# Optimization experiments

Hardware: AMD Instinct MI355X
Metric: run time of the kernel (lower is better)

## Reference

```python
import jax, jax.numpy as jnp
import numpy as np
import math

E = 1024   # embed_size
H = 16     # heads arg (actual per-'head' dim due to source's reshape quirk)
G = E // H # 64 head-groups (treated as heads in the source code)
FF = 4 * E


def setup_inputs() -> dict:
    key = jax.random.key(0)
    ks = jax.random.split(key, 12)
    s = 1.0 / math.sqrt(E)
    inp = {
        'x': jax.random.normal(ks[0], (2, 1024, E), dtype=jnp.float32),
        # linear weights stored as (in, out); torch Linear computes x @ W.T + b
        'Wq': jax.random.uniform(ks[1], (E, E), jnp.float32, -s, s),
        'Wk': jax.random.uniform(ks[2], (E, E), jnp.float32, -s, s),
        'Wv': jax.random.uniform(ks[3], (E, E), jnp.float32, -s, s),
        'Wo': jax.random.uniform(ks[4], (E, E), jnp.float32, -s, s),
        'bo': jax.random.uniform(ks[5], (E,), jnp.float32, -s, s),
        'W1': jax.random.uniform(ks[6], (E, FF), jnp.float32, -s, s),
        'b1': jax.random.uniform(ks[7], (FF,), jnp.float32, -s, s),
        'W2': jax.random.uniform(ks[8], (FF, E), jnp.float32, -1.0 / math.sqrt(FF), 1.0 / math.sqrt(FF)),
        'b2': jax.random.uniform(ks[9], (E,), jnp.float32, -s, s),
        'g1': jnp.ones((E,), jnp.float32), 'be1': jnp.zeros((E,), jnp.float32),
        'g2': jnp.ones((E,), jnp.float32), 'be2': jnp.zeros((E,), jnp.float32),
    }
    return inp


def _layernorm(x, g, b, eps=1e-5):
    mu = jnp.mean(x, axis=-1, keepdims=True)
    var = jnp.mean(jnp.square(x - mu), axis=-1, keepdims=True)
    return (x - mu) * jax.lax.rsqrt(var + eps) * g + b


def reference(x, Wq, Wk, Wv, Wo, bo, W1, b1, W2, b2, g1, be1, g2, be2):
    B, S, _ = x.shape
    # QKV projections; faithful to source: split E into (G=E//H groups, H dims),
    # group axis acts as the 'head' axis, per-head dim is H, scale = sqrt(H).
    def split(t):  # [B,S,E] -> [B,G,S,H]
        return t.reshape(B, S, G, H).transpose(0, 2, 1, 3)
    q = split(x @ Wq)
    k = split(x @ Wk)
    v = split(x @ Wv)
    att = jnp.einsum('bgsh,bgth->bgst', q, k) / math.sqrt(H)
    causal = jnp.tril(jnp.ones((S, S), dtype=bool))  # mask==1 above diag -> -inf
    att = jnp.where(causal, att, -jnp.inf)
    att = jax.nn.softmax(att, axis=-1)
    y = jnp.einsum('bgst,bgth->bgsh', att, v)          # [B,G,S,H]
    y = y.transpose(0, 2, 1, 3).reshape(B, S, E)
    attn_out = y @ Wo + bo
    # dropout is identity at inference
    x = _layernorm(attn_out + x, g1, be1)
    ff = jax.nn.relu(x @ W1 + b1) @ W2 + b2
    x = _layernorm(ff + x, g2, be2)
    return x
```

## Files before the change

kernel.cpp:

```cpp
#include <hip/hip_runtime.h>
#include <hip/hip_bf16.h>
#include <math.h>


#define E_DIM 1024
#define S_LEN 1024
#define B_SZ  2
#define G_HEADS 64
#define H_DIM 16
#define FF_DIM 4096
#define M_ROWS (B_SZ * S_LEN)
#define QKV_N  (3 * E_DIM)

#define QSCALE 0.36067376022224085f

#define VT_STRIDE 72
#define VT_BUF    1224

using bf16x8 = __attribute__((ext_vector_type(8))) short;
using f32x4  = __attribute__((ext_vector_type(4))) float;
using f32x16 = __attribute__((ext_vector_type(16))) float;
using ushort8 = __attribute__((ext_vector_type(8))) unsigned short;

static __device__ __forceinline__ unsigned short f2bf(float f) {
    union { float f; unsigned int u; } x; x.f = f;
    unsigned int r = x.u + 0x7fff + ((x.u >> 16) & 1);
    return (unsigned short)(r >> 16);
}
static __device__ __forceinline__ unsigned int pack2(float a, float b) {
    union { __hip_bfloat162 h; unsigned int u; } c;
    c.h = __float22bfloat162_rn(float2{a, b});
    return c.u;
}

__global__ __launch_bounds__(256) void cast_kernel(
    const float* __restrict__ X, unsigned short* __restrict__ Xb)
{
    const size_t i = ((size_t)blockIdx.x * 256 + threadIdx.x) * 8;
    float4 a = *(const float4*)(X + i);
    float4 b = *(const float4*)(X + i + 4);
    ushort8 o;
    o[0] = f2bf(a.x); o[1] = f2bf(a.y); o[2] = f2bf(a.z); o[3] = f2bf(a.w);
    o[4] = f2bf(b.x); o[5] = f2bf(b.y); o[6] = f2bf(b.z); o[7] = f2bf(b.w);
    *(ushort8*)(Xb + i) = o;
}

__global__ __launch_bounds__(256) void transpose_cast4_kernel(
    const float* __restrict__ W0, const float* __restrict__ W1_,
    const float* __restrict__ W2_, const float* __restrict__ W3_,
    unsigned short* __restrict__ Wt012, unsigned short* __restrict__ Wt3)
{
    __shared__ float tile[32][33];
    const int z = blockIdx.z;
    const float* W = (z == 0) ? W0 : (z == 1) ? W1_ : (z == 2) ? W2_ : W3_;
    unsigned short* Wo = (z < 3) ? (Wt012 + (size_t)z * E_DIM * E_DIM) : Wt3;
    const int n0 = blockIdx.x * 32, k0 = blockIdx.y * 32;
    const int t = threadIdx.x;
    const int r = t >> 3;
    const int c = (t & 7) * 4;

    float4 v = *(const float4*)(W + (size_t)(k0 + r) * E_DIM + n0 + c);
    tile[r][c] = v.x; tile[r][c + 1] = v.y; tile[r][c + 2] = v.z; tile[r][c + 3] = v.w;
    __syncthreads();

    ushort4 o;
    o.x = f2bf(tile[c + 0][r]); o.y = f2bf(tile[c + 1][r]);
    o.z = f2bf(tile[c + 2][r]); o.w = f2bf(tile[c + 3][r]);
    *(ushort4*)(Wo + (size_t)(n0 + r) * E_DIM + k0 + c) = o;
}

__global__ __launch_bounds__(256) void transpose_cast_ff_kernel(
    const float* __restrict__ W1_, const float* __restrict__ W2_,
    unsigned short* __restrict__ W1t, unsigned short* __restrict__ W2t)
{
    __shared__ float tile[32][33];
    const int z = blockIdx.z;
    const float* W = z ? W2_ : W1_;
    unsigned short* Wt = z ? W2t : W1t;
    const int N = z ? E_DIM : FF_DIM;
    const int K = z ? FF_DIM : E_DIM;
    const int n0 = (z ? blockIdx.y : blockIdx.x) * 32;
    const int k0 = (z ? blockIdx.x : blockIdx.y) * 32;
    const int t = threadIdx.x;
    const int r = t >> 3;
    const int c = (t & 7) * 4;

    float4 v = *(const float4*)(W + (size_t)(k0 + r) * N + n0 + c);
    tile[r][c] = v.x; tile[r][c + 1] = v.y; tile[r][c + 2] = v.z; tile[r][c + 3] = v.w;
    __syncthreads();

    ushort4 o;
    o.x = f2bf(tile[c + 0][r]); o.y = f2bf(tile[c + 1][r]);
    o.z = f2bf(tile[c + 2][r]); o.w = f2bf(tile[c + 3][r]);
    *(ushort4*)(Wt + (size_t)(n0 + r) * K + k0 + c) = o;
}

template<int ACT, int OUTBF, int SCALEQ>
__global__ __launch_bounds__(256) void gemm_mfma(
    const unsigned short* __restrict__ A,
    const unsigned short* __restrict__ Bt,
    const float* __restrict__ bias,
    float* __restrict__ C0, float* __restrict__ C1,
    unsigned short* __restrict__ Cb,
    int Krow, int Kchunk, int ldc)
{
    __shared__ __align__(16) unsigned short lds[2][12288];

    const int tid  = threadIdx.x;
    const int wave = tid >> 6;
    const int lane = tid & 63;
    const int wr = wave >> 1;
    const int wc = wave & 1;
    const int row0 = blockIdx.y * 128;
    const int col0 = blockIdx.x * 64;
    const int kbase = blockIdx.z * Kchunk;

    const int lr = lane & 15;
    const int lk = (lane >> 4) * 8;

    const int srow = (lane >> 2);
    const int scol = (lane & 3) * 8;

    f32x4 acc[4][2] = {};

    auto STAGE1 = [&](unsigned short* dstA, unsigned short* dstB, int k0) {
        #pragma unroll
        for (int i = 0; i < 2; ++i) {
            const int ci = wave + i * 4;
            const unsigned short* src =
                A + (size_t)(row0 + ci * 16 + srow) * Krow + k0 + scol;
            __builtin_amdgcn_global_load_lds(
                (const __attribute__((address_space(1))) void*)src,
                (__attribute__((address_space(3))) void*)(dstA + ci * 512),
                16, 0, 0);
        }
        {
            const unsigned short* src =
                Bt + (size_t)(col0 + wave * 16 + srow) * Krow + k0 + scol;
            __builtin_amdgcn_global_load_lds(
                (const __attribute__((address_space(1))) void*)src,
                (__attribute__((address_space(3))) void*)(dstB + wave * 512),
                16, 0, 0);
        }
    };
    auto STAGE = [&](int buf, int k0) {
        STAGE1(&lds[buf][0],    &lds[buf][4096],  k0);
        STAGE1(&lds[buf][6144], &lds[buf][10240], k0 + 32);
    };
    auto COMPUTE = [&](int buf, int sub) {
        const unsigned short* As = &lds[buf][sub * 6144];
        const unsigned short* Bs = As + 4096;
        bf16x8 a[4], b[2];
        #pragma unroll
        for (int mi = 0; mi < 4; ++mi)
            a[mi] = *(const bf16x8*)(As + (wr * 64 + mi * 16 + lr) * 32 + lk);
        #pragma unroll
        for (int ni = 0; ni < 2; ++ni)
            b[ni] = *(const bf16x8*)(Bs + (wc * 32 + ni * 16 + lr) * 32 + lk);
        #pragma unroll
        for (int mi = 0; mi < 4; ++mi)
            #pragma unroll
            for (int ni = 0; ni < 2; ++ni)
                acc[mi][ni] = __builtin_amdgcn_mfma_f32_16x16x32_bf16(
                    a[mi], b[ni], acc[mi][ni], 0, 0, 0);
    };

    const int nt = Kchunk >> 6;

    STAGE(0, kbase);
    asm volatile("s_waitcnt vmcnt(0)" ::: "memory");
    __builtin_amdgcn_s_barrier();

    int cur = 0;
    for (int t = 0; t < nt; ++t) {
        if (t + 1 < nt) STAGE(cur ^ 1, kbase + (t + 1) * 64);
        COMPUTE(cur, 0);
        COMPUTE(cur, 1);
        asm volatile("s_waitcnt vmcnt(0)" ::: "memory");
        __builtin_amdgcn_s_barrier();
        cur ^= 1;
    }

    float* Cw = blockIdx.z ? C1 : C0;
    #pragma unroll
    for (int mi = 0; mi < 4; ++mi) {
        #pragma unroll
        for (int ni = 0; ni < 2; ++ni) {
            const int cc  = col0 + wc * 32 + ni * 16 + (lane & 15);
            const int rr0 = row0 + wr * 64 + mi * 16 + ((lane >> 4) << 2);
            const float bv = bias ? bias[cc] : 0.f;
            #pragma unroll
            for (int j = 0; j < 4; ++j) {
                float v = acc[mi][ni][j] + bv;
                if (ACT == 1) v = fmaxf(v, 0.f);
                if (SCALEQ && cc < E_DIM) v *= QSCALE;
                if (OUTBF) Cb[(size_t)(rr0 + j) * ldc + cc] = f2bf(v);
                else       Cw[(size_t)(rr0 + j) * ldc + cc] = v;
            }
        }
    }
}

__global__ __launch_bounds__(256) void attn_kernel(
    const unsigned short* __restrict__ qkv, unsigned short* __restrict__ Yb)
{
    __shared__ __align__(16) unsigned short Ks[2][1024];
    __shared__ __align__(16) unsigned short Vt[2][VT_BUF];

    const int bi = blockIdx.x >> 7;
    const int bg = blockIdx.x & 127;
    const int g  = bg & (G_HEADS - 1);
    const int b  = bg >> 6;
    const int tid  = threadIdx.x;
    const int lane = tid & 63;
    const int l31  = lane & 31;
    const int hi   = lane >> 5;
    const int wv   = tid >> 6;
    const int tokb = b * S_LEN;

    const int cblk = 28 - 4 * bi;
    const int q0   = (cblk + wv) * 32;
    const int qrow = q0 + l31;
    const int nt64 = (cblk + 4) >> 1;

    const bf16x8 qf = *(const bf16x8*)(
        qkv + (size_t)(tokb + qrow) * QKV_N + g * H_DIM + hi * 8);

    f32x16 acc = {};
    const f32x16 fz = {};

    const int kv  = tid >> 7;
    const int h64 = (tid >> 6) & 1;
    const int skey  = h64 * 32 + (lane >> 1);
    const int shalf = lane & 1;
    const size_t sgo = (size_t)(g * H_DIM + (1 + kv) * E_DIM + shalf * 8);

    auto STAGE = [&](int buf, int t64, ushort8& vreg) {
        const unsigned short* src =
            qkv + (size_t)(tokb + t64 * 64 + skey) * QKV_N + sgo;
        if (kv == 0) {
            __builtin_amdgcn_global_load_lds(
                (const __attribute__((address_space(1))) void*)src,
                (__attribute__((address_space(3))) void*)(&Ks[buf][h64 * 512]),
                16, 0, 0);
        } else {
            vreg = *(const ushort8*)src;
        }
    };
    auto WRITE_V = [&](int buf, const ushort8& vreg) {
        if (kv == 1) {
            #pragma unroll
            for (int j = 0; j < 8; ++j)
                Vt[buf][(shalf * 8 + j) * VT_STRIDE + skey] = vreg[j];
        }
    };

    const int vrow = (l31 == 16) ? 16 : (l31 & 15);

    auto PROCESS = [&](int cur, int sub, int t0) {
        const bf16x8 kf = *(const bf16x8*)(&Ks[cur][(sub * 32 + l31) * 16 + hi * 8]);
        __builtin_amdgcn_s_setprio(1);
        f32x16 s = __builtin_amdgcn_mfma_f32_32x32x16_bf16(kf, qf, fz, 0, 0, 0);
        __builtin_amdgcn_s_setprio(0);

        float pq[16];
        if (t0 == q0) {
            #pragma unroll
            for (int r = 0; r < 16; ++r) {
                const int key = t0 + (r & 3) + 8 * (r >> 2) + 4 * hi;
                pq[r] = (key > qrow) ? 0.f : exp2f(s[r]);
            }
        } else {
            #pragma unroll
            for (int r = 0; r < 16; ++r) pq[r] = exp2f(s[r]);
        }

        unsigned int cw[8];
        #pragma unroll
        for (int r2 = 0; r2 < 8; ++r2) cw[r2] = pack2(pq[2 * r2], pq[2 * r2 + 1]);

        union { uint4 u; bf16x8 v; } pf0, pf1;
        {
            unsigned int a = cw[0], c = cw[2];
            asm volatile("v_permlane32_swap_b32 %0, %1" : "+v"(a), "+v"(c));
            pf0.u.x = a; pf0.u.z = c;
        }
        {
            unsigned int a = cw[1], c = cw[3];
            asm volatile("v_permlane32_swap_b32 %0, %1" : "+v"(a), "+v"(c));
            pf0.u.y = a; pf0.u.w = c;
        }
        {
            unsigned int a = cw[4], c = cw[6];
            asm volatile("v_permlane32_swap_b32 %0, %1" : "+v"(a), "+v"(c));
            pf1.u.x = a; pf1.u.z = c;
        }
        {
            unsigned int a = cw[5], c = cw[7];
            asm volatile("v_permlane32_swap_b32 %0, %1" : "+v"(a), "+v"(c));
            pf1.u.y = a; pf1.u.w = c;
        }

        const unsigned short* vbase =
            &Vt[cur][vrow * VT_STRIDE + sub * 32 + hi * 8];
        const bf16x8 vb0 = *(const bf16x8*)(vbase);
        const bf16x8 vb1 = *(const bf16x8*)(vbase + 16);

        __builtin_amdgcn_s_setprio(1);
        acc = __builtin_amdgcn_mfma_f32_32x32x16_bf16(pf0.v, vb0, acc, 0, 0, 0);
        acc = __builtin_amdgcn_mfma_f32_32x32x16_bf16(pf1.v, vb1, acc, 0, 0, 0);
        __builtin_amdgcn_s_setprio(0);
    };

    ushort8 vreg = {};
    STAGE(0, 0, vreg);
    if (kv == 1) {
        const int vt = tid - 128;
        Vt[vt >> 6][16 * VT_STRIDE + (vt & 63)] = 0x3F80;
    }
    WRITE_V(0, vreg);
    __syncthreads();

    int cur = 0;
    for (int t = 0; t < nt64; ++t) {
        ushort8 vnext = {};
        const bool more = (t + 1 < nt64);
        if (more) STAGE(cur ^ 1, t + 1, vnext);
        #pragma unroll
        for (int sub = 0; sub < 2; ++sub) {
            const int t0 = t * 64 + sub * 32;
            if (t0 <= q0) PROCESS(cur, sub, t0);
        }
        if (more) WRITE_V(cur ^ 1, vnext);
        asm volatile("s_waitcnt vmcnt(0) lgkmcnt(0)" ::: "memory");
        __builtin_amdgcn_s_barrier();
        cur ^= 1;
    }

    float linv[16];
    #pragma unroll
    for (int r = 0; r < 16; ++r) {
        const float lr_ = __shfl(acc[r], (hi << 5) + 16);
        linv[r] = __builtin_amdgcn_rcpf(lr_);
    }
    if (l31 < H_DIM) {
        #pragma unroll
        for (int r = 0; r < 16; ++r) {
            const int q = (r & 3) + 8 * (r >> 2) + 4 * hi;
            Yb[(size_t)(tokb + q0 + q) * E_DIM + g * H_DIM + l31] =
                f2bf(acc[r] * linv[r]);
        }
    }
}

__global__ __launch_bounds__(256) void add_ln2_kernel(
    const float* __restrict__ P0, const float* __restrict__ P1,
    const float* __restrict__ bias, const float* __restrict__ resid,
    const float* __restrict__ g, const float* __restrict__ be,
    float* __restrict__ O, unsigned short* __restrict__ Ob)
{
    const int row = blockIdx.x;
    const size_t base = (size_t)row * E_DIM;
    const int tid = threadIdx.x;

    float v[4];
    float s = 0.f;
    #pragma unroll
    for (int i = 0; i < 4; ++i) {
        int c = tid + i * 256;
        v[i] = P0[base + c] + P1[base + c] + bias[c] + resid[base + c];
        s += v[i];
    }

    __shared__ float red[256];
    red[tid] = s; __syncthreads();
    for (int st = 128; st >= 1; st >>= 1) {
        if (tid < st) red[tid] += red[tid + st];
        __syncthreads();
    }
    const float mu = red[0] * (1.f / E_DIM);
    __syncthreads();

    float s2 = 0.f;
    #pragma unroll
    for (int i = 0; i < 4; ++i) { float d = v[i] - mu; s2 += d * d; }
    red[tid] = s2; __syncthreads();
    for (int st = 128; st >= 1; st >>= 1) {
        if (tid < st) red[tid] += red[tid + st];
        __syncthreads();
    }
    const float rs = rsqrtf(red[0] * (1.f / E_DIM) + 1e-5f);

    #pragma unroll
    for (int i = 0; i < 4; ++i) {
        int c = tid + i * 256;
        float o = (v[i] - mu) * rs * g[c] + be[c];
        O[base + c] = o;
        if (Ob) Ob[base + c] = f2bf(o);
    }
}

extern "C" void kernel_launch(void* const* d_in, const int* in_sizes, int n_in,
                              void* d_out, int out_size, void* d_ws, size_t ws_size,
                              hipStream_t stream)
{
    const float* x  = (const float*)d_in[0];
    const float* Wq = (const float*)d_in[1];
    const float* Wk = (const float*)d_in[2];
    const float* Wv = (const float*)d_in[3];
    const float* Wo = (const float*)d_in[4];
    const float* bo = (const float*)d_in[5];
    const float* W1 = (const float*)d_in[6];
    const float* b1 = (const float*)d_in[7];
    const float* W2 = (const float*)d_in[8];
    const float* b2 = (const float*)d_in[9];
    const float* g1  = (const float*)d_in[10];
    const float* be1 = (const float*)d_in[11];
    const float* g2  = (const float*)d_in[12];
    const float* be2 = (const float*)d_in[13];

    char* W = (char*)d_ws;
    const size_t MB = 1024 * 1024;
    unsigned short* xb   = (unsigned short*)(W + 0 * MB);
    unsigned short* Wqkt = (unsigned short*)(W + 4 * MB);
    unsigned short* qkvb = (unsigned short*)(W + 10 * MB);
    unsigned short* yb   = (unsigned short*)(W + 22 * MB);
    unsigned short* Wot  = (unsigned short*)(W + 26 * MB);
    float* P_o0          = (float*)(W + 4 * MB);
    float* P_o1          = (float*)(W + 12 * MB);
    unsigned short* x1b  = (unsigned short*)(W + 20 * MB);
    float* x1            = (float*)(W + 28 * MB);
    unsigned short* W1t  = (unsigned short*)(W + 36 * MB);
    unsigned short* W2t  = (unsigned short*)(W + 44 * MB);
    unsigned short* ff1b = (unsigned short*)(W + 0 * MB);
    float* P_f1          = (float*)(W + 16 * MB);
    float* out           = (float*)d_out;

    dim3 blk(256);

    cast_kernel<<<dim3((M_ROWS * E_DIM) / (256 * 8)), blk, 0, stream>>>(x, xb);
    transpose_cast4_kernel<<<dim3(32, 32, 4), blk, 0, stream>>>(Wq, Wk, Wv, Wo, Wqkt, Wot);
    transpose_cast_ff_kernel<<<dim3(128, 32, 2), blk, 0, stream>>>(W1, W2, W1t, W2t);
    gemm_mfma<0, 1, 1><<<dim3(QKV_N / 64, M_ROWS / 128, 1), blk, 0, stream>>>(
        xb, Wqkt, nullptr, nullptr, nullptr, qkvb, E_DIM, E_DIM, QKV_N);
    attn_kernel<<<dim3(B_SZ * G_HEADS * 8), blk, 0, stream>>>(qkvb, yb);
    gemm_mfma<0, 0, 0><<<dim3(E_DIM / 64, M_ROWS / 128, 2), blk, 0, stream>>>(
        yb, Wot, nullptr, P_o0, P_o1, nullptr, E_DIM, E_DIM / 2, E_DIM);
    add_ln2_kernel<<<dim3(M_ROWS), blk, 0, stream>>>(P_o0, P_o1, bo, x, g1, be1, x1, x1b);
    gemm_mfma<1, 1, 0><<<dim3(FF_DIM / 64, M_ROWS / 128, 1), blk, 0, stream>>>(
        x1b, W1t, b1, nullptr, nullptr, ff1b, E_DIM, E_DIM, FF_DIM);
    gemm_mfma<0, 0, 0><<<dim3(E_DIM / 64, M_ROWS / 128, 2), blk, 0, stream>>>(
        ff1b, W2t, nullptr, out, P_f1, nullptr, FF_DIM, FF_DIM / 2, E_DIM);
    add_ln2_kernel<<<dim3(M_ROWS), blk, 0, stream>>>(out, P_f1, b2, x1, g2, be2, out, nullptr);
}
```

Before: 162.7 us.

## Merge prep kernels and drop LDS staging in attention for direct global loads

Three casting and transposing kernels become one prep kernel that dispatches on a flat block index, saving two launches. The attention kernel no longer stages K and V tiles through double-buffered shared memory with barriers. Each wave now walks only its own causal range of 32-key steps, loading K as a vector from global memory with a one-step prefetch and gathering V with scalar strided global loads. This removes block-level synchronisation and LDS traffic, but the many uncoalesced 2-byte V loads may cost more than they save.

After: 229.8 us. 1.41x slower.

```diff
diff --git a/kernel.cpp b/kernel.cpp
--- a/kernel.cpp
+++ b/kernel.cpp
@@ -14,9 +14,6 @@
 
 #define QSCALE 0.36067376022224085f
 
-#define VT_STRIDE 72
-#define VT_BUF    1224
-
 using bf16x8 = __attribute__((ext_vector_type(8))) short;
 using f32x4  = __attribute__((ext_vector_type(4))) float;
 using f32x16 = __attribute__((ext_vector_type(16))) float;
@@ -33,54 +30,48 @@
     return c.u;
 }
 
-__global__ __launch_bounds__(256) void cast_kernel(
-    const float* __restrict__ X, unsigned short* __restrict__ Xb)
+__global__ __launch_bounds__(256) void prep_kernel(
+    const float* __restrict__ x,
+    const float* __restrict__ Wq, const float* __restrict__ Wk,
+    const float* __restrict__ Wv, const float* __restrict__ Wo,
+    const float* __restrict__ W1_, const float* __restrict__ W2_,
+    unsigned short* __restrict__ xb, unsigned short* __restrict__ Wqkt,
+    unsigned short* __restrict__ Wot, unsigned short* __restrict__ W1t,
+    unsigned short* __restrict__ W2t)
 {
-    const size_t i = ((size_t)blockIdx.x * 256 + threadIdx.x) * 8;
-    float4 a = *(const float4*)(X + i);
-    float4 b = *(const float4*)(X + i + 4);
-    ushort8 o;
-    o[0] = f2bf(a.x); o[1] = f2bf(a.y); o[2] = f2bf(a.z); o[3] = f2bf(a.w);
-    o[4] = f2bf(b.x); o[5] = f2bf(b.y); o[6] = f2bf(b.z); o[7] = f2bf(b.w);
-    *(ushort8*)(Xb + i) = o;
-}
-
-__global__ __launch_bounds__(256) void transpose_cast4_kernel(
-    const float* __restrict__ W0, const float* __restrict__ W1_,
-    const float* __restrict__ W2_, const float* __restrict__ W3_,
-    unsigned short* __restrict__ Wt012, unsigned short* __restrict__ Wt3)
-{
+    const int id = blockIdx.x;
+    if (id < 1024) {
+        const size_t i = ((size_t)id * 256 + threadIdx.x) * 8;
+        float4 a = *(const float4*)(x + i);
+        float4 b = *(const float4*)(x + i + 4);
+        ushort8 o;
+        o[0] = f2bf(a.x); o[1] = f2bf(a.y); o[2] = f2bf(a.z); o[3] = f2bf(a.w);
+        o[4] = f2bf(b.x); o[5] = f2bf(b.y); o[6] = f2bf(b.z); o[7] = f2bf(b.w);
+        *(ushort8*)(xb + i) = o;
+        return;
+    }
+
     __shared__ float tile[32][33];
-    const int z = blockIdx.z;
-    const float* W = (z == 0) ? W0 : (z == 1) ? W1_ : (z == 2) ? W2_ : W3_;
-    unsigned short* Wo = (z < 3) ? (Wt012 + (size_t)z * E_DIM * E_DIM) : Wt3;
-    const int n0 = blockIdx.x * 32, k0 = blockIdx.y * 32;
-    const int t = threadIdx.x;
-    const int r = t >> 3;
-    const int c = (t & 7) * 4;
-
-    float4 v = *(const float4*)(W + (size_t)(k0 + r) * E_DIM + n0 + c);
-    tile[r][c] = v.x; tile[r][c + 1] = v.y; tile[r][c + 2] = v.z; tile[r][c + 3] = v.w;
-    __syncthreads();
-
-    ushort4 o;
-    o.x = f2bf(tile[c + 0][r]); o.y = f2bf(tile[c + 1][r]);
-    o.z = f2bf(tile[c + 2][r]); o.w = f2bf(tile[c + 3][r]);
-    *(ushort4*)(Wo + (size_t)(n0 + r) * E_DIM + k0 + c) = o;
-}
-
-__global__ __launch_bounds__(256) void transpose_cast_ff_kernel(
-    const float* __restrict__ W1_, const float* __restrict__ W2_,
-    unsigned short* __restrict__ W1t, unsigned short* __restrict__ W2t)
-{
-    __shared__ float tile[32][33];
-    const int z = blockIdx.z;
-    const float* W = z ? W2_ : W1_;
-    unsigned short* Wt = z ? W2t : W1t;
-    const int N = z ? E_DIM : FF_DIM;
-    const int K = z ? FF_DIM : E_DIM;
-    const int n0 = (z ? blockIdx.y : blockIdx.x) * 32;
-    const int k0 = (z ? blockIdx.x : blockIdx.y) * 32;
+    const float* W; unsigned short* Wt; int N, K, n0, k0;
+    if (id < 5120) {
+        const int q = id - 1024;
+        const int z = q >> 10;
+        W  = (z == 0) ? Wq : (z == 1) ? Wk : (z == 2) ? Wv : Wo;
+        Wt = (z < 3) ? (Wqkt + (size_t)z * E_DIM * E_DIM) : Wot;
+        N = E_DIM; K = E_DIM;
+        n0 = (q & 31) * 32; k0 = ((q >> 5) & 31) * 32;
+    } else {
+        const int q = id - 5120;
+        const int z = q >> 12;
+        const int qx = q & 4095;
+        const int bx = qx & 127, by = qx >> 7;
+        W  = z ? W2_ : W1_;
+        Wt = z ? W2t : W1t;
+        N  = z ? E_DIM : FF_DIM;
+        K  = z ? FF_DIM : E_DIM;
+        n0 = (z ? by : bx) * 32;
+        k0 = (z ? bx : by) * 32;
+    }
     const int t = threadIdx.x;
     const int r = t >> 3;
     const int c = (t & 7) * 4;
@@ -204,9 +195,6 @@
 __global__ __launch_bounds__(256) void attn_kernel(
     const unsigned short* __restrict__ qkv, unsigned short* __restrict__ Yb)
 {
-    __shared__ __align__(16) unsigned short Ks[2][1024];
-    __shared__ __align__(16) unsigned short Vt[2][VT_BUF];
-
     const int bi = blockIdx.x >> 7;
     const int bg = blockIdx.x & 127;
     const int g  = bg & (G_HEADS - 1);
@@ -221,44 +209,42 @@
     const int cblk = 28 - 4 * bi;
     const int q0   = (cblk + wv) * 32;
     const int qrow = q0 + l31;
-    const int nt64 = (cblk + 4) >> 1;
+    const int nsub = (q0 >> 5) + 1;
 
     const bf16x8 qf = *(const bf16x8*)(
         qkv + (size_t)(tokb + qrow) * QKV_N + g * H_DIM + hi * 8);
 
+    const unsigned short* kbase =
+        qkv + (size_t)(tokb + l31) * QKV_N + g * H_DIM + E_DIM + hi * 8;
+    const size_t KSTEP = (size_t)32 * QKV_N;
+
+    const bool isl = (l31 == 16);
+    const int vcol = l31 & 15;
+    const unsigned short* vbase =
+        qkv + (size_t)tokb * QKV_N + g * H_DIM + 2 * E_DIM + vcol;
+
     f32x16 acc = {};
     const f32x16 fz = {};
 
-    const int kv  = tid >> 7;
-    const int h64 = (tid >> 6) & 1;
-    const int skey  = h64 * 32 + (lane >> 1);
-    const int shalf = lane & 1;
-    const size_t sgo = (size_t)(g * H_DIM + (1 + kv) * E_DIM + shalf * 8);
-
-    auto STAGE = [&](int buf, int t64, ushort8& vreg) {
-        const unsigned short* src =
-            qkv + (size_t)(tokb + t64 * 64 + skey) * QKV_N + sgo;
-        if (kv == 0) {
-            __builtin_amdgcn_global_load_lds(
-                (const __attribute__((address_space(1))) void*)src,
-                (__attribute__((address_space(3))) void*)(&Ks[buf][h64 * 512]),
-                16, 0, 0);
-        } else {
-            vreg = *(const ushort8*)src;
-        }
-    };
-    auto WRITE_V = [&](int buf, const ushort8& vreg) {
-        if (kv == 1) {
-            #pragma unroll
-            for (int j = 0; j < 8; ++j)
-                Vt[buf][(shalf * 8 + j) * VT_STRIDE + skey] = vreg[j];
-        }
-    };
-
-    const int vrow = (l31 == 16) ? 16 : (l31 & 15);
-
-    auto PROCESS = [&](int cur, int sub, int t0) {
-        const bf16x8 kf = *(const bf16x8*)(&Ks[cur][(sub * 32 + l31) * 16 + hi * 8]);
+    bf16x8 kf = *(const bf16x8*)(kbase);
+
+    for (int t = 0; t < nsub; ++t) {
+        const int t0 = t * 32;
+
+        bf16x8 kf_next = kf;
+        if (t + 1 < nsub)
+            kf_next = *(const bf16x8*)(kbase + (size_t)(t + 1) * KSTEP);
+
+        union { unsigned short s2[8]; bf16x8 v; } vb0, vb1;
+        #pragma unroll
+        for (int e = 0; e < 8; ++e) {
+            const int k0_ = t0 + hi * 8 + e;
+            vb0.s2[e] = isl ? (unsigned short)0x3F80
+                            : vbase[(size_t)k0_ * QKV_N];
+            vb1.s2[e] = isl ? (unsigned short)0x3F80
+                            : vbase[(size_t)(k0_ + 16) * QKV_N];
+        }
+
         __builtin_amdgcn_s_setprio(1);
         f32x16 s = __builtin_amdgcn_mfma_f32_32x32x16_bf16(kf, qf, fz, 0, 0, 0);
         __builtin_amdgcn_s_setprio(0);
@@ -301,40 +287,12 @@
             pf1.u.y = a; pf1.u.w = c;
         }
 
-        const unsigned short* vbase =
-            &Vt[cur][vrow * VT_STRIDE + sub * 32 + hi * 8];
-        const bf16x8 vb0 = *(const bf16x8*)(vbase);
-        const bf16x8 vb1 = *(const bf16x8*)(vbase + 16);
-
         __builtin_amdgcn_s_setprio(1);
-        acc = __builtin_amdgcn_mfma_f32_32x32x16_bf16(pf0.v, vb0, acc, 0, 0, 0);
-        acc = __builtin_amdgcn_mfma_f32_32x32x16_bf16(pf1.v, vb1, acc, 0, 0, 0);
+        acc = __builtin_amdgcn_mfma_f32_32x32x16_bf16(pf0.v, vb0.v, acc, 0, 0, 0);
+        acc = __builtin_amdgcn_mfma_f32_32x32x16_bf16(pf1.v, vb1.v, acc, 0, 0, 0);
         __builtin_amdgcn_s_setprio(0);
-    };
-
-    ushort8 vreg = {};
-    STAGE(0, 0, vreg);
-    if (kv == 1) {
-        const int vt = tid - 128;
-        Vt[vt >> 6][16 * VT_STRIDE + (vt & 63)] = 0x3F80;
-    }
-    WRITE_V(0, vreg);
-    __syncthreads();
-
-    int cur = 0;
-    for (int t = 0; t < nt64; ++t) {
-        ushort8 vnext = {};
-        const bool more = (t + 1 < nt64);
-        if (more) STAGE(cur ^ 1, t + 1, vnext);
-        #pragma unroll
-        for (int sub = 0; sub < 2; ++sub) {
-            const int t0 = t * 64 + sub * 32;
-            if (t0 <= q0) PROCESS(cur, sub, t0);
-        }
-        if (more) WRITE_V(cur ^ 1, vnext);
-        asm volatile("s_waitcnt vmcnt(0) lgkmcnt(0)" ::: "memory");
-        __builtin_amdgcn_s_barrier();
-        cur ^= 1;
+
+        kf = kf_next;
     }
 
     float linv[16];
@@ -438,9 +396,8 @@
 
     dim3 blk(256);
 
-    cast_kernel<<<dim3((M_ROWS * E_DIM) / (256 * 8)), blk, 0, stream>>>(x, xb);
-    transpose_cast4_kernel<<<dim3(32, 32, 4), blk, 0, stream>>>(Wq, Wk, Wv, Wo, Wqkt, Wot);
-    transpose_cast_ff_kernel<<<dim3(128, 32, 2), blk, 0, stream>>>(W1, W2, W1t, W2t);
+    prep_kernel<<<dim3(13312), blk, 0, stream>>>(
+        x, Wq, Wk, Wv, Wo, W1, W2, xb, Wqkt, Wot, W1t, W2t);
     gemm_mfma<0, 1, 1><<<dim3(QKV_N / 64, M_ROWS / 128, 1), blk, 0, stream>>>(
         xb, Wqkt, nullptr, nullptr, nullptr, qkvb, E_DIM, E_DIM, QKV_N);
     attn_kernel<<<dim3(B_SZ * G_HEADS * 8), blk, 0, stream>>>(qkvb, yb);
```
